# Optimization experiments

Hardware: AMD Instinct MI355X
Metric: run time of the kernel (lower is better)

## Reference

```python
import jax, jax.numpy as jnp
import numpy as np


def setup_inputs() -> dict:
    key = jax.random.key(0)
    ks = jax.random.split(key, 5)
    B, L, I, H = 512, 200, 512, 512
    x = jax.random.normal(ks[0], (B, L, I), dtype=jnp.float32)
    att = jax.random.uniform(ks[1], (L, B), dtype=jnp.float32)  # attention scores per (time, batch)
    h0 = jnp.zeros((B, H), dtype=jnp.float32)
    s = 1.0 / np.sqrt(H)
    w_ih = jax.random.uniform(ks[2], (3 * H, I), minval=-s, maxval=s, dtype=jnp.float32)
    w_hh = jax.random.uniform(ks[3], (3 * H, H), minval=-s, maxval=s, dtype=jnp.float32)
    b_ih = jnp.zeros((3 * H,), dtype=jnp.float32)
    b_hh = jnp.zeros((3 * H,), dtype=jnp.float32)
    return {"x": x, "att": att, "h0": h0, "w_ih": w_ih, "w_hh": w_hh, "b_ih": b_ih, "b_hh": b_hh}


def reference(x, att, h0, w_ih, w_hh, b_ih, b_hh):
    # x: [B,L,I] (batch_first), att: [L,B], h0: [B,H]
    # Precompute all input-hidden projections in one batched GEMM: [L,B,3H]
    gx_all = jnp.einsum('bli,gi->lbg', x, w_ih) + b_ih

    def step(h, inp):
        gx, w = inp                              # gx: [B,3H], w: [B]
        gh = h @ w_hh.T + b_hh                   # [B,3H]
        xr, xz, xn = jnp.split(gx, 3, axis=-1)
        hr, hz, hn = jnp.split(gh, 3, axis=-1)
        r = jax.nn.sigmoid(xr + hr)
        z = jax.nn.sigmoid(xz + hz)
        n = jnp.tanh(xn + r * hn)
        h_o = (1.0 - z) * n + z * h              # torch GRUCell update
        w = w[:, None]
        h_new = (1.0 - w) * h + w * h_o          # attention-weighted interpolation
        return h_new, h_new

    hx, out = jax.lax.scan(step, h0, (gx_all, att))
    out = jnp.moveaxis(out, 0, 1)  # [B,L,H] (batch_first output)
    return out, hx
```

## Files before the change

### kernel.cpp

```cpp
#include <hip/hip_runtime.h>
#include <hip/hip_fp16.h>

#define LDIM 200
#define BDIM 512
#define IDIM 512
#define HDIM 512
#define GDIM 1536
#define NGRP 16
#define NCOL 16

typedef _Float16 f16x8 __attribute__((ext_vector_type(8)));
typedef _Float16 f16x4 __attribute__((ext_vector_type(4)));
typedef float    f32x4 __attribute__((ext_vector_type(4)));

__global__ __launch_bounds__(256) void k_init(
    unsigned int* __restrict__ flags, const float* __restrict__ h0,
    _Float16* __restrict__ hb)
{
    int i = blockIdx.x * 256 + threadIdx.x;
    if (i < NGRP * NCOL) flags[i] = 0;
    if (i < BDIM * HDIM) hb[i] = (_Float16)h0[i];
}

__global__ __launch_bounds__(256) void k_pack_wfi(
    const float* __restrict__ w, f16x8* __restrict__ wf)
{
    int u = blockIdx.x * 256 + threadIdx.x;
    if (u >= (GDIM / 16) * 16 * 64) return;
    const int lane = u & 63;
    const int kk   = (u >> 6) & 15;
    const int ntg  = u >> 10;
    const int n = ntg * 16 + (lane & 15);
    const int k = kk * 32 + (lane >> 4) * 8;
    const float* src = w + (size_t)n * IDIM + k;
    f16x8 v;
    #pragma unroll
    for (int j = 0; j < 8; ++j) v[j] = (_Float16)src[j];
    wf[u] = v;
}

__global__ __launch_bounds__(256) void k_pack_wfh(
    const float* __restrict__ w, f16x8* __restrict__ wf)
{
    int u = blockIdx.x * 256 + threadIdx.x;
    if (u >= NCOL * 6 * 16 * 64) return;
    const int lane = u & 63;
    const int kk   = (u >> 6) & 15;
    const int cw   = u >> 10;
    const int wv   = cw % 6;
    const int c    = cw / 6;
    const int n_local = wv * 16 + (lane & 15);
    const int gate    = n_local >> 5;
    const int j_local = n_local & 31;
    const int n = gate * 512 + c * 32 + j_local;
    const int k = kk * 32 + (lane >> 4) * 8;
    const float* src = w + (size_t)n * HDIM + k;
    f16x8 v;
    #pragma unroll
    for (int j = 0; j < 8; ++j) v[j] = (_Float16)src[j];
    wf[u] = v;
}

__global__ __launch_bounds__(256) void k_gemm_gx(
    const float* __restrict__ x, const f16x8* __restrict__ wfi,
    const float* __restrict__ bih, _Float16* __restrict__ gx)
{
    const int bid  = blockIdx.x;
    const int xcd  = bid & 7;
    const int slot = bid >> 3;
    const int gl   = slot / 12;
    const int j    = slot - gl * 12;
    const int m0   = (xcd * 100 + gl) * 128;
    const int n0   = j * 128;

    const int t = threadIdx.x;
    const int w = t >> 6;
    const int l = t & 63;
    const int mw = m0 + w * 32;
    const int ko = (l >> 4) * 8;

    const int r0 = mw + (l & 15);
    const int r1 = r0 + 16;
    const float* a0 = x + ((size_t)(r0 & 511) * LDIM + (r0 >> 9)) * IDIM;
    const float* a1 = x + ((size_t)(r1 & 511) * LDIM + (r1 >> 9)) * IDIM;
    const f16x8* bp = wfi + (size_t)(j * 8) * 1024 + l;

    f32x4 acc[2][8] = {};

    for (int kk = 0; kk < 16; ++kk) {
        const int k = kk * 32 + ko;
        f16x8 af[2];
        {
            const float4 v0 = *reinterpret_cast<const float4*>(a0 + k);
            const float4 v1 = *reinterpret_cast<const float4*>(a0 + k + 4);
            const float4 v2 = *reinterpret_cast<const float4*>(a1 + k);
            const float4 v3 = *reinterpret_cast<const float4*>(a1 + k + 4);
            af[0][0] = (_Float16)v0.x; af[0][1] = (_Float16)v0.y;
            af[0][2] = (_Float16)v0.z; af[0][3] = (_Float16)v0.w;
            af[0][4] = (_Float16)v1.x; af[0][5] = (_Float16)v1.y;
            af[0][6] = (_Float16)v1.z; af[0][7] = (_Float16)v1.w;
            af[1][0] = (_Float16)v2.x; af[1][1] = (_Float16)v2.y;
            af[1][2] = (_Float16)v2.z; af[1][3] = (_Float16)v2.w;
            af[1][4] = (_Float16)v3.x; af[1][5] = (_Float16)v3.y;
            af[1][6] = (_Float16)v3.z; af[1][7] = (_Float16)v3.w;
        }
        const f16x8* bk = bp + kk * 64;
        #pragma unroll
        for (int nt = 0; nt < 8; ++nt) {
            const f16x8 bf = bk[(size_t)nt * 1024];
            acc[0][nt] = __builtin_amdgcn_mfma_f32_16x16x32_f16(af[0], bf, acc[0][nt], 0, 0, 0);
            acc[1][nt] = __builtin_amdgcn_mfma_f32_16x16x32_f16(af[1], bf, acc[1][nt], 0, 0, 0);
        }
    }

    #pragma unroll
    for (int nt = 0; nt < 8; ++nt) {
        const int n = n0 + nt * 16 + (l & 15);
        const float bv = bih[n];
        #pragma unroll
        for (int mt = 0; mt < 2; ++mt) {
            #pragma unroll
            for (int r = 0; r < 4; ++r) {
                const int m = mw + mt * 16 + (l >> 4) * 4 + r;
                gx[(size_t)m * GDIM + n] = (_Float16)(acc[mt][nt][r] + bv);
            }
        }
    }
}

__global__ __launch_bounds__(384) void k_recur(
    const _Float16* __restrict__ gx, const float* __restrict__ att,
    const float* __restrict__ h0, const f16x8* __restrict__ wfh,
    const float* __restrict__ bhh, _Float16* __restrict__ hb,
    unsigned int* __restrict__ flags, float* __restrict__ out,
    float* __restrict__ hx)
{
    const int bid = blockIdx.x;
    const int g = bid >> 4;
    const int c = bid & 15;
    const int t = threadIdx.x;
    const int w = t >> 6;
    const int l = t & 63;

    __shared__ __align__(16) _Float16 h16[32 * 512];
    __shared__ float ghs[96][33];

    f16x8 B[16];
    {
        const f16x8* p = wfh + (size_t)(c * 6 + w) * 1024 + l;
        #pragma unroll
        for (int kk = 0; kk < 16; ++kk) B[kk] = p[kk * 64];
    }

    const int i  = t >> 3;
    const int j4 = (t & 7) * 4;

    float bhr[4], bhz[4], bhn[4], hv[4];
    if (t < 256) {
        const float4 r4 = *(const float4*)(bhh + c * 32 + j4);
        const float4 z4 = *(const float4*)(bhh + 512 + c * 32 + j4);
        const float4 n4 = *(const float4*)(bhh + 1024 + c * 32 + j4);
        bhr[0]=r4.x; bhr[1]=r4.y; bhr[2]=r4.z; bhr[3]=r4.w;
        bhz[0]=z4.x; bhz[1]=z4.y; bhz[2]=z4.z; bhz[3]=z4.w;
        bhn[0]=n4.x; bhn[1]=n4.y; bhn[2]=n4.z; bhn[3]=n4.w;
        const float4 h4 = *(const float4*)(h0 + (size_t)(g * 32 + i) * 512 + c * 32 + j4);
        hv[0]=h4.x; hv[1]=h4.y; hv[2]=h4.z; hv[3]=h4.w;
    }

    const unsigned int* fline = flags + g * 16;
    unsigned int* myflag = flags + g * 16 + c;

    const int ib = (l >> 4) * 4;
    const int nl = w * 16 + (l & 15);
    const int k8 = (l >> 4) * 8;
    const int rr0 = l & 15;
    const int rr1 = rr0 + 16;

    int rd = 0;
    for (int s = 0; s < LDIM; ++s) {
        f16x4 gr_r = {}, gr_z = {}, gr_n = {};
        float av = 0.f;
        if (t < 256) {
            const _Float16* gp = gx + ((size_t)s * BDIM + g * 32 + i) * GDIM + c * 32 + j4;
            gr_r = *(const f16x4*)(gp);
            gr_z = *(const f16x4*)(gp + 512);
            gr_n = *(const f16x4*)(gp + 1024);
            av = att[(size_t)s * BDIM + g * 32 + i];
        }

        if (s > 0 && w == 0) {
            const unsigned int* fp = fline + (l & 15);
            unsigned int fv;
            do {
                asm volatile("global_load_dword %0, %1, off sc0 sc1\n\t"
                             "s_waitcnt vmcnt(0)"
                             : "=v"(fv) : "v"(fp) : "memory");
            } while (fv < (unsigned int)s);
        }
        __syncthreads();

        if (t < 256) {
            const unsigned long long* hsrc = (const unsigned long long*)
                (hb + (size_t)rd * (BDIM * HDIM) + (size_t)g * 32 * 512);
            unsigned long long vv[16];
            #pragma unroll
            for (int q = 0; q < 16; ++q) {
                asm volatile("global_load_dwordx2 %0, %1, off sc0 sc1"
                             : "=v"(vv[q]) : "v"(hsrc + q * 256 + t));
            }
            asm volatile("s_waitcnt vmcnt(0)" ::: "memory");
            __builtin_amdgcn_sched_barrier(0);
            #pragma unroll
            for (int q = 0; q < 16; ++q) {
                const int idx = q * 256 + t;
                const int row = idx >> 7;
                const int c8  = idx & 127;
                const int byte = (row * 1024 + c8 * 8) ^ ((row & 7) << 4);
                *(unsigned long long*)((char*)h16 + byte) = vv[q];
            }
        }
        __syncthreads();

        f32x4 acc0 = {0.f, 0.f, 0.f, 0.f};
        f32x4 acc1 = {0.f, 0.f, 0.f, 0.f};
        #pragma unroll
        for (int kk = 0; kk < 16; ++kk) {
            const int kb = kk * 64 + k8 * 2;
            const int b0 = (rr0 * 1024 + kb) ^ ((rr0 & 7) << 4);
            const int b1 = (rr1 * 1024 + kb) ^ ((rr1 & 7) << 4);
            const f16x8 a0 = *(const f16x8*)((const char*)h16 + b0);
            const f16x8 a1 = *(const f16x8*)((const char*)h16 + b1);
            acc0 = __builtin_amdgcn_mfma_f32_16x16x32_f16(a0, B[kk], acc0, 0, 0, 0);
            acc1 = __builtin_amdgcn_mfma_f32_16x16x32_f16(a1, B[kk], acc1, 0, 0, 0);
        }
        #pragma unroll
        for (int q = 0; q < 4; ++q) {
            ghs[nl][ib + q]      = acc0[q];
            ghs[nl][16 + ib + q] = acc1[q];
        }
        __syncthreads();

        const int wr = (rd == 2) ? 0 : rd + 1;
        if (t < 256) {
            float o[4];
            f16x4 hp;
            #pragma unroll
            for (int q = 0; q < 4; ++q) {
                const int jl = j4 + q;
                const float hr = ghs[jl][i]      + bhr[q];
                const float hz = ghs[32 + jl][i] + bhz[q];
                const float hn = ghs[64 + jl][i] + bhn[q];
                const float h  = hv[q];
                const float rg = 1.f / (1.f + __expf(-((float)gr_r[q] + hr)));
                const float zg = 1.f / (1.f + __expf(-((float)gr_z[q] + hz)));
                const float ng = tanhf((float)gr_n[q] + rg * hn);
                const float ho = (1.f - zg) * ng + zg * h;
                const float hnew = (1.f - av) * h + av * ho;
                hv[q] = hnew;
                o[q] = hnew;
                hp[q] = (_Float16)hnew;
            }
            *(float4*)(out + ((size_t)(g * 32 + i) * LDIM + s) * HDIM + c * 32 + j4)
                = *(float4*)o;
            union { f16x4 v; unsigned long long u; } pk; pk.v = hp;
            _Float16* hd = hb + (size_t)wr * (BDIM * HDIM)
                         + (size_t)(g * 32 + i) * 512 + c * 32 + j4;
            asm volatile("global_store_dwordx2 %0, %1, off sc0 sc1"
                         :: "v"(hd), "v"(pk.u) : "memory");
        }
        asm volatile("s_waitcnt vmcnt(0)" ::: "memory");
        __syncthreads();
        if (t == 0) {
            unsigned int fv = (unsigned int)(s + 1);
            asm volatile("global_store_dword %0, %1, off sc0 sc1"
                         :: "v"(myflag), "v"(fv) : "memory");
        }
        rd = wr;
    }

    if (t < 256) {
        float o[4] = {hv[0], hv[1], hv[2], hv[3]};
        *(float4*)(hx + (size_t)(g * 32 + i) * 512 + c * 32 + j4) = *(float4*)o;
    }
}

extern "C" void kernel_launch(void* const* d_in, const int* in_sizes, int n_in,
                              void* d_out, int out_size, void* d_ws, size_t ws_size,
                              hipStream_t stream)
{
    const float* x   = (const float*)d_in[0];
    const float* att = (const float*)d_in[1];
    const float* h0  = (const float*)d_in[2];
    const float* wih = (const float*)d_in[3];
    const float* whh = (const float*)d_in[4];
    const float* bih = (const float*)d_in[5];
    const float* bhh = (const float*)d_in[6];

    float* out = (float*)d_out;
    float* hx  = out + (size_t)BDIM * LDIM * HDIM;

    char* ws = (char*)d_ws;
    f16x8*        wfA   = (f16x8*)ws;
    unsigned int* flags = (unsigned int*)(ws + 0x180000);
    _Float16*     hb    = (_Float16*)(ws + 0x190000);
    _Float16*     gx    = (_Float16*)(ws + 0x310000);

    k_init<<<1024, 256, 0, stream>>>(flags, h0, hb);
    k_pack_wfi<<<384, 256, 0, stream>>>(wih, wfA);
    k_gemm_gx<<<9600, 256, 0, stream>>>(x, wfA, bih, gx);
    k_pack_wfh<<<384, 256, 0, stream>>>(whh, wfA);
    k_recur<<<256, 384, 0, stream>>>(gx, att, h0, wfA, bhh, hb, flags, out, hx);
}
```

Baseline: 1.530 ms.

## Stage GEMM A tile in LDS, prefetch next-step gx, defer output store

The input-projection GEMM now gives each block a 64-row by 512-column tile. The block converts x to fp16 once into a swizzled LDS buffer and reuses it across four waves, which avoids re-reading and re-converting x for every 128-column tile. In the recurrence kernel, the gx and att values for the next timestep are loaded before the MFMA phase to hide their latency. The gh scratch is transposed so each thread can read its gates as float4 vectors. The output store is moved after the flag publish, so the global wait covers only the h store and the out write stays off the critical path. The cost is higher LDS use in the GEMM (64KB per block, launch bounds set to 2 blocks per CU) and more live registers in the recurrence.

```diff
diff --git a/kernel.cpp b/kernel.cpp
--- a/kernel.cpp
+++ b/kernel.cpp
@@ -61,67 +61,77 @@
     wf[u] = v;
 }
 
-__global__ __launch_bounds__(256) void k_gemm_gx(
+__global__ __launch_bounds__(256, 2) void k_gemm_gx(
     const float* __restrict__ x, const f16x8* __restrict__ wfi,
     const float* __restrict__ bih, _Float16* __restrict__ gx)
 {
     const int bid  = blockIdx.x;
     const int xcd  = bid & 7;
     const int slot = bid >> 3;
-    const int gl   = slot / 12;
-    const int j    = slot - gl * 12;
-    const int m0   = (xcd * 100 + gl) * 128;
-    const int n0   = j * 128;
-
-    const int t = threadIdx.x;
-    const int w = t >> 6;
-    const int l = t & 63;
-    const int mw = m0 + w * 32;
-    const int ko = (l >> 4) * 8;
-
-    const int r0 = mw + (l & 15);
-    const int r1 = r0 + 16;
-    const float* a0 = x + ((size_t)(r0 & 511) * LDIM + (r0 >> 9)) * IDIM;
-    const float* a1 = x + ((size_t)(r1 & 511) * LDIM + (r1 >> 9)) * IDIM;
-    const f16x8* bp = wfi + (size_t)(j * 8) * 1024 + l;
-
-    f32x4 acc[2][8] = {};
+    const int gl   = slot / 3;
+    const int ng   = slot % 3;
+    const int m0   = (xcd * 200 + gl) * 64;
+    const int n0   = ng * 512;
+
+    const int t   = threadIdx.x;
+    const int wid = t >> 6;
+    const int l   = t & 63;
+
+    __shared__ __align__(16) _Float16 As[64 * 512];
+
+    {
+        const int r  = t >> 2;
+        const int k0 = (t & 3) * 128;
+        const int m  = m0 + r;
+        const float* src = x + ((size_t)(m & 511) * LDIM + (m >> 9)) * IDIM + k0;
+        #pragma unroll
+        for (int jj = 0; jj < 16; ++jj) {
+            const float4 v0 = *(const float4*)(src + jj * 8);
+            const float4 v1 = *(const float4*)(src + jj * 8 + 4);
+            f16x8 hq;
+            hq[0] = (_Float16)v0.x; hq[1] = (_Float16)v0.y;
+            hq[2] = (_Float16)v0.z; hq[3] = (_Float16)v0.w;
+            hq[4] = (_Float16)v1.x; hq[5] = (_Float16)v1.y;
+            hq[6] = (_Float16)v1.z; hq[7] = (_Float16)v1.w;
+            const int byte = (r * 1024 + (k0 + jj * 8) * 2) ^ ((r & 7) << 4);
+            *(f16x8*)((char*)As + byte) = hq;
+        }
+    }
+    __syncthreads();
+
+    const f16x8* bp = wfi + (size_t)((ng * 4 + wid) * 8) * 1024 + l;
+    const int kb8   = (l >> 4) * 16;
+    const int rbase = l & 15;
+
+    f32x4 acc[4][8] = {};
 
     for (int kk = 0; kk < 16; ++kk) {
-        const int k = kk * 32 + ko;
-        f16x8 af[2];
-        {
-            const float4 v0 = *reinterpret_cast<const float4*>(a0 + k);
-            const float4 v1 = *reinterpret_cast<const float4*>(a0 + k + 4);
-            const float4 v2 = *reinterpret_cast<const float4*>(a1 + k);
-            const float4 v3 = *reinterpret_cast<const float4*>(a1 + k + 4);
-            af[0][0] = (_Float16)v0.x; af[0][1] = (_Float16)v0.y;
-            af[0][2] = (_Float16)v0.z; af[0][3] = (_Float16)v0.w;
-            af[0][4] = (_Float16)v1.x; af[0][5] = (_Float16)v1.y;
-            af[0][6] = (_Float16)v1.z; af[0][7] = (_Float16)v1.w;
-            af[1][0] = (_Float16)v2.x; af[1][1] = (_Float16)v2.y;
-            af[1][2] = (_Float16)v2.z; af[1][3] = (_Float16)v2.w;
-            af[1][4] = (_Float16)v3.x; af[1][5] = (_Float16)v3.y;
-            af[1][6] = (_Float16)v3.z; af[1][7] = (_Float16)v3.w;
+        f16x8 a[4];
+        #pragma unroll
+        for (int mt = 0; mt < 4; ++mt) {
+            const int r = mt * 16 + rbase;
+            const int byte = (r * 1024 + kk * 64 + kb8) ^ ((r & 7) << 4);
+            a[mt] = *(const f16x8*)((const char*)As + byte);
         }
         const f16x8* bk = bp + kk * 64;
         #pragma unroll
         for (int nt = 0; nt < 8; ++nt) {
             const f16x8 bf = bk[(size_t)nt * 1024];
-            acc[0][nt] = __builtin_amdgcn_mfma_f32_16x16x32_f16(af[0], bf, acc[0][nt], 0, 0, 0);
-            acc[1][nt] = __builtin_amdgcn_mfma_f32_16x16x32_f16(af[1], bf, acc[1][nt], 0, 0, 0);
+            #pragma unroll
+            for (int mt = 0; mt < 4; ++mt)
+                acc[mt][nt] = __builtin_amdgcn_mfma_f32_16x16x32_f16(a[mt], bf, acc[mt][nt], 0, 0, 0);
         }
     }
 
     #pragma unroll
     for (int nt = 0; nt < 8; ++nt) {
-        const int n = n0 + nt * 16 + (l & 15);
+        const int n = n0 + wid * 128 + nt * 16 + (l & 15);
         const float bv = bih[n];
         #pragma unroll
-        for (int mt = 0; mt < 2; ++mt) {
+        for (int mt = 0; mt < 4; ++mt) {
             #pragma unroll
             for (int r = 0; r < 4; ++r) {
-                const int m = mw + mt * 16 + (l >> 4) * 4 + r;
+                const int m = m0 + mt * 16 + (l >> 4) * 4 + r;
                 gx[(size_t)m * GDIM + n] = (_Float16)(acc[mt][nt][r] + bv);
             }
         }
@@ -143,7 +153,7 @@
     const int l = t & 63;
 
     __shared__ __align__(16) _Float16 h16[32 * 512];
-    __shared__ float ghs[96][33];
+    __shared__ float ghsT[32][100];
 
     f16x8 B[16];
     {
@@ -176,18 +186,18 @@
     const int rr0 = l & 15;
     const int rr1 = rr0 + 16;
 
+    f16x4 cr = {}, cz = {}, cn = {};
+    float ca = 0.f;
+    if (t < 256) {
+        const _Float16* gp = gx + ((size_t)(g * 32 + i)) * GDIM + c * 32 + j4;
+        cr = *(const f16x4*)(gp);
+        cz = *(const f16x4*)(gp + 512);
+        cn = *(const f16x4*)(gp + 1024);
+        ca = att[g * 32 + i];
+    }
+
     int rd = 0;
     for (int s = 0; s < LDIM; ++s) {
-        f16x4 gr_r = {}, gr_z = {}, gr_n = {};
-        float av = 0.f;
-        if (t < 256) {
-            const _Float16* gp = gx + ((size_t)s * BDIM + g * 32 + i) * GDIM + c * 32 + j4;
-            gr_r = *(const f16x4*)(gp);
-            gr_z = *(const f16x4*)(gp + 512);
-            gr_n = *(const f16x4*)(gp + 1024);
-            av = att[(size_t)s * BDIM + g * 32 + i];
-        }
-
         if (s > 0 && w == 0) {
             const unsigned int* fp = fline + (l & 15);
             unsigned int fv;
@@ -219,6 +229,17 @@
                 *(unsigned long long*)((char*)h16 + byte) = vv[q];
             }
         }
+
+        f16x4 nr = {}, nz = {}, nn2 = {};
+        float na = 0.f;
+        if (t < 256) {
+            const int sn = (s < LDIM - 1) ? s + 1 : s;
+            const _Float16* gp = gx + ((size_t)sn * BDIM + g * 32 + i) * GDIM + c * 32 + j4;
+            nr  = *(const f16x4*)(gp);
+            nz  = *(const f16x4*)(gp + 512);
+            nn2 = *(const f16x4*)(gp + 1024);
+            na  = att[(size_t)sn * BDIM + g * 32 + i];
+        }
         __syncthreads();
 
         f32x4 acc0 = {0.f, 0.f, 0.f, 0.f};
@@ -235,46 +256,54 @@
         }
         #pragma unroll
         for (int q = 0; q < 4; ++q) {
-            ghs[nl][ib + q]      = acc0[q];
-            ghs[nl][16 + ib + q] = acc1[q];
+            ghsT[ib + q][nl]      = acc0[q];
+            ghsT[16 + ib + q][nl] = acc1[q];
         }
         __syncthreads();
 
         const int wr = (rd == 2) ? 0 : rd + 1;
+        float o[4];
         if (t < 256) {
-            float o[4];
+            const float4 ghr = *(const float4*)&ghsT[i][j4];
+            const float4 ghz = *(const float4*)&ghsT[i][32 + j4];
+            const float4 ghn = *(const float4*)&ghsT[i][64 + j4];
+            const float hrr[4] = {ghr.x, ghr.y, ghr.z, ghr.w};
+            const float hzz[4] = {ghz.x, ghz.y, ghz.z, ghz.w};
+            const float hnn[4] = {ghn.x, ghn.y, ghn.z, ghn.w};
             f16x4 hp;
             #pragma unroll
             for (int q = 0; q < 4; ++q) {
-                const int jl = j4 + q;
-                const float hr = ghs[jl][i]      + bhr[q];
-                const float hz = ghs[32 + jl][i] + bhz[q];
-                const float hn = ghs[64 + jl][i] + bhn[q];
+                const float hr = hrr[q] + bhr[q];
+                const float hz = hzz[q] + bhz[q];
+                const float hn = hnn[q] + bhn[q];
                 const float h  = hv[q];
-                const float rg = 1.f / (1.f + __expf(-((float)gr_r[q] + hr)));
-                const float zg = 1.f / (1.f + __expf(-((float)gr_z[q] + hz)));
-                const float ng = tanhf((float)gr_n[q] + rg * hn);
+                const float rg = 1.f / (1.f + __expf(-((float)cr[q] + hr)));
+                const float zg = 1.f / (1.f + __expf(-((float)cz[q] + hz)));
+                const float ng = tanhf((float)cn[q] + rg * hn);
                 const float ho = (1.f - zg) * ng + zg * h;
-                const float hnew = (1.f - av) * h + av * ho;
+                const float hnew = (1.f - ca) * h + ca * ho;
                 hv[q] = hnew;
                 o[q] = hnew;
                 hp[q] = (_Float16)hnew;
             }
-            *(float4*)(out + ((size_t)(g * 32 + i) * LDIM + s) * HDIM + c * 32 + j4)
-                = *(float4*)o;
             union { f16x4 v; unsigned long long u; } pk; pk.v = hp;
             _Float16* hd = hb + (size_t)wr * (BDIM * HDIM)
                          + (size_t)(g * 32 + i) * 512 + c * 32 + j4;
             asm volatile("global_store_dwordx2 %0, %1, off sc0 sc1"
                          :: "v"(hd), "v"(pk.u) : "memory");
-        }
-        asm volatile("s_waitcnt vmcnt(0)" ::: "memory");
+            asm volatile("s_waitcnt vmcnt(0)" ::: "memory");
+        }
         __syncthreads();
         if (t == 0) {
             unsigned int fv = (unsigned int)(s + 1);
             asm volatile("global_store_dword %0, %1, off sc0 sc1"
                          :: "v"(myflag), "v"(fv) : "memory");
         }
+        if (t < 256) {
+            *(float4*)(out + ((size_t)(g * 32 + i) * LDIM + s) * HDIM + c * 32 + j4)
+                = *(float4*)o;
+        }
+        cr = nr; cz = nz; cn = nn2; ca = na;
         rd = wr;
     }
 
@@ -307,7 +336,7 @@
 
     k_init<<<1024, 256, 0, stream>>>(flags, h0, hb);
     k_pack_wfi<<<384, 256, 0, stream>>>(wih, wfA);
-    k_gemm_gx<<<9600, 256, 0, stream>>>(x, wfA, bih, gx);
+    k_gemm_gx<<<4800, 256, 0, stream>>>(x, wfA, bih, gx);
     k_pack_wfh<<<384, 256, 0, stream>>>(whh, wfA);
     k_recur<<<256, 384, 0, stream>>>(gx, att, h0, wfA, bhh, hb, flags, out, hx);
 }
```

After: 1.360 ms. 11.1% less time.
